# Performance work log

Hardware: AMD Instinct MI355X
Metric: run time of the kernel (lower is better)

Reference implementation:

```python
import jax, jax.numpy as jnp
import numpy as np
import math

MID = 48       # mid_channels
HEADS = 4      # num_heads
POS = 16       # mid_channels // 3 (row/col positional channels)


def _unfold(x, p):
    """nn.Unfold with kernel p, padding p//2: (..., H, W) -> (..., p, p, H, W)."""
    H, W = x.shape[-2], x.shape[-1]
    pad = p // 2
    xp = jnp.pad(x, [(0, 0)] * (x.ndim - 2) + [(pad, pad), (pad, pad)])
    return jnp.stack(
        [jnp.stack([xp[..., k:k + H, l:l + W] for l in range(p)], axis=-3)
         for k in range(p)], axis=-4)


def _pe_mlp(idx, w1, b1, g, b, w2, b2):
    """Conv2d(1->16,1x1) -> LayerNorm(16) -> Swish -> Conv2d(16->POS,1x1) on scalar coords."""
    t = idx.reshape(-1, 1)                         # (N,1)
    h = t @ w1.T + b1                              # (N,16)
    mu = jnp.mean(h, -1, keepdims=True)
    var = jnp.var(h, -1, keepdims=True)
    h = (h - mu) * jax.lax.rsqrt(var + 1e-5) * g + b
    h = h * jax.nn.sigmoid(h)                      # Swish
    e = h @ w2.T + b2                              # (N,POS)
    return e.reshape(idx.shape + (e.shape[-1],))   # (V,P,P,POS)


def setup_inputs() -> dict:
    key = jax.random.key(0)
    ks = jax.random.split(key, 32)
    B, Cin, G, H, W, P, Cout = 2, 32, 4, 28, 28, 7, 64

    def n(k, shp, s=0.05):
        return jax.random.normal(k, shp, dtype=jnp.float32) * s

    inp = {"x": jax.random.normal(ks[0], (B, Cin, G, H, W), dtype=jnp.float32)}
    inp["Wq"] = n(ks[1], (MID * HEADS, Cin)); inp["bq"] = n(ks[2], (MID * HEADS,))
    inp["Wk"] = n(ks[3], (MID * HEADS, Cin)); inp["bk"] = n(ks[4], (MID * HEADS,))
    inp["Wv"] = n(ks[5], (MID * HEADS, Cin)); inp["bv"] = n(ks[6], (MID * HEADS,))
    inp["Wout"] = n(ks[7], (Cout, MID * HEADS)); inp["bout"] = n(ks[8], (Cout,))
    inp["row_w1"] = n(ks[9], (16, 1)); inp["row_b1"] = n(ks[10], (16,))
    inp["row_ln_g"] = jnp.ones((16,), jnp.float32); inp["row_ln_b"] = jnp.zeros((16,), jnp.float32)
    inp["row_w2"] = n(ks[11], (POS, 16)); inp["row_b2"] = n(ks[12], (POS,))
    inp["col_w1"] = n(ks[13], (16, 1)); inp["col_b1"] = n(ks[14], (16,))
    inp["col_ln_g"] = jnp.ones((16,), jnp.float32); inp["col_ln_b"] = jnp.zeros((16,), jnp.float32)
    inp["col_w2"] = n(ks[15], (POS, 16)); inp["col_b2"] = n(ks[16], (POS,))
    inp["group_emb"] = n(ks[17], (G, MID - 2 * POS))
    # rotated relative spatial positions, normalized to [-1, 1]
    lin = np.linspace(-1.0, 1.0, P).astype(np.float32)
    r = np.repeat(lin[:, None], P, 1)
    c = np.repeat(lin[None, :], P, 0)
    rows, cols = [], []
    for v in range(G):
        th = v * math.pi / 2.0
        rows.append(math.cos(th) * r - math.sin(th) * c)
        cols.append(math.sin(th) * r + math.cos(th) * c)
    inp["row_indices"] = jnp.asarray(np.stack(rows, 0))
    inp["col_indices"] = jnp.asarray(np.stack(cols, 0))
    # acted relative group positions for cyclic group C4
    ar = np.arange(G)
    gi = (ar[:, None, None] + ar[None, None, :] - ar[None, :, None]) % G
    inp["g_indices"] = jnp.asarray(gi, dtype=jnp.int32)
    return inp


def _forward(x, Wq, bq, Wk, bk, Wv, bv, Wout, bout,
             row_w1, row_b1, row_ln_g, row_ln_b, row_w2, row_b2,
             col_w1, col_b1, col_ln_g, col_ln_b, col_w2, col_b2,
             group_emb, row_indices, col_indices, g_indices):
    B, Cin, G, H, W = x.shape
    P = row_indices.shape[-1]
    sqn = jnp.sqrt(jnp.float32(Cin))

    def proj(Wm, bm):  # 1x1 Conv3d -> (B, MID, HEADS, G, H, W)
        y = jnp.einsum('oi,bigyx->bogyx', Wm, x) + bm[None, :, None, None, None]
        return y.reshape(B, MID, HEADS, G, H, W)

    q = proj(Wq, bq)
    k = proj(Wk, bk)
    v = proj(Wv, bv)
    k_loc = _unfold(k, P)   # (B, MID, HEADS, G, P, P, H, W)
    v_loc = _unfold(v, P)

    content = jnp.einsum('bchgij,bchmklij->bhgijmkl', q, k_loc)
    row_e = _pe_mlp(row_indices, row_w1, row_b1, row_ln_g, row_ln_b, row_w2, row_b2)
    col_e = _pe_mlp(col_indices, col_w1, col_b1, col_ln_g, col_ln_b, col_w2, col_b2)
    row_s = jnp.einsum('bchgij,vklc->bhvgijkl', q[:, :POS], row_e)
    col_s = jnp.einsum('bchgij,vklc->bhvgijkl', q[:, POS:2 * POS], col_e)
    g_e = group_emb[g_indices]                              # (V, G, M, gdim)
    g_s = jnp.einsum('bchgij,vgmc->bhvgijm', q[:, 2 * POS:], g_e)

    # scores: (b, h, v, g, i, j, m, k, l)
    scores = (row_s[:, :, :, :, :, :, None] + col_s[:, :, :, :, :, :, None]
              + g_s[..., None, None] + content[:, :, None]) / sqn

    # mask patch positions that fall outside the image (-inf -> prob 0)
    valid = _unfold(jnp.ones((H, W), jnp.float32), P)       # (P, P, H, W)
    valid = jnp.transpose(valid, (2, 3, 0, 1))[None, None, None, None, :, :, None, :, :]
    scores = jnp.where(valid > 0.5, scores, -jnp.inf)

    shp = scores.shape
    probs = jax.nn.softmax(scores.reshape(shp[:-3] + (-1,)), axis=-1).reshape(shp)

    o = jnp.einsum('bhvgijmkl,bchmklij->bchvij', probs, v_loc)  # (B, MID, HEADS, V, H, W)
    o = o.reshape(B, MID * HEADS, G, H, W)
    return jnp.einsum('oi,bivyx->bovyx', Wout, o) + bout[None, :, None, None, None]


def reference(x, Wq, bq, Wk, bk, Wv, bv, Wout, bout,
              row_w1, row_b1, row_ln_g, row_ln_b, row_w2, row_b2,
              col_w1, col_b1, col_ln_g, col_ln_b, col_w2, col_b2,
              group_emb, row_indices, col_indices, g_indices):
    return _forward(x, Wq, bq, Wk, bk, Wv, bv, Wout, bout,
                    row_w1, row_b1, row_ln_g, row_ln_b, row_w2, row_b2,
                    col_w1, col_b1, col_ln_g, col_ln_b, col_w2, col_b2,
                    group_emb, row_indices, col_indices, g_indices)
```

## Files before the change

### kernel.cpp

```cpp
#include <hip/hip_runtime.h>
#include <math.h>

#define Bb   2
#define CIN  32
#define Gg   4
#define NH   4
#define Hh   28
#define Ww   28
#define HW   784
#define Pp   7
#define PP   49
#define MID  48
#define COUT 64
#define OC   192

#define QOFF  0
#define KOFF  1204224
#define VOFF  2408448
#define OOFF  3612672

#define KSCALE 0.2550611135387359f

#define VP1F 3360

__device__ unsigned g_peT2[Gg * PP * 16];
__device__ unsigned g_geT2[8 * 64];
__device__ float    g_WT2[OC * COUT];

typedef _Float16 h2f __attribute__((ext_vector_type(2)));

__device__ __forceinline__ unsigned packh2(float a, float b) {
    auto r = __builtin_amdgcn_cvt_pkrtz(a, b);
    return __builtin_bit_cast(unsigned, r);
}

__device__ __forceinline__ float fdot2(unsigned a, unsigned b, float c) {
    return __builtin_amdgcn_fdot2(__builtin_bit_cast(h2f, a),
                                  __builtin_bit_cast(h2f, b), c, false);
}

__device__ __forceinline__ float exp2_fast(float x) {
    float r;
    asm("v_exp_f32 %0, %1" : "=v"(r) : "v"(x));
    return r;
}

__global__ __launch_bounds__(192) void qkvpe_kernel(const float* __restrict__ x,
    const float* __restrict__ Wq, const float* __restrict__ bq,
    const float* __restrict__ Wk, const float* __restrict__ bk,
    const float* __restrict__ Wv, const float* __restrict__ bv,
    const float* row_w1, const float* row_b1,
    const float* row_g,  const float* row_bb,
    const float* row_w2, const float* row_b2,
    const float* col_w1, const float* col_b1,
    const float* col_g,  const float* col_bb,
    const float* col_w2, const float* col_b2,
    const float* row_idx, const float* col_idx,
    const float* group_emb, const int* g_indices,
    const float* Wout,
    float* __restrict__ ws)
{
    __shared__ float xs[CIN * 16];
    __shared__ float wtmp[16 * 193];
    int tid = threadIdx.x;
    if (blockIdx.x == Bb * Gg * Hh * 2) {
        for (int t = tid; t < 2 * Gg * PP; t += 192) {
            int half = t / (Gg * PP);
            int n    = t - half * (Gg * PP);
            int v = n / PP, kl = n % PP;
            const float* w1 = half ? col_w1 : row_w1;
            const float* b1 = half ? col_b1 : row_b1;
            const float* lg = half ? col_g  : row_g;
            const float* lb = half ? col_bb : row_bb;
            const float* w2 = half ? col_w2 : row_w2;
            const float* b2 = half ? col_b2 : row_b2;
            float tv = half ? col_idx[n] : row_idx[n];

            float hb[16];
            float mean = 0.f;
            for (int k = 0; k < 16; k++) { hb[k] = tv * w1[k] + b1[k]; mean += hb[k]; }
            mean *= (1.f / 16.f);
            float var = 0.f;
            for (int k = 0; k < 16; k++) { float d = hb[k] - mean; var += d * d; }
            var *= (1.f / 16.f);
            float inv = 1.f / sqrtf(var + 1e-5f);
            for (int k = 0; k < 16; k++) {
                float hn = (hb[k] - mean) * inv * lg[k] + lb[k];
                hb[k] = hn / (1.f + expf(-hn));
            }
            float accv[16];
            for (int p = 0; p < 16; p++) {
                float acc = b2[p];
                for (int k = 0; k < 16; k++) acc += hb[k] * w2[p * 16 + k];
                accv[p] = acc * KSCALE;
            }
            for (int i2 = 0; i2 < 8; i2++)
                g_peT2[(v * PP + kl) * 16 + half * 8 + i2] =
                    packh2(accv[2 * i2], accv[2 * i2 + 1]);
        }
        for (int t = tid; t < 64; t += 192) {
            int gi = g_indices[t];
            for (int i2 = 0; i2 < 8; i2++)
                g_geT2[i2 * 64 + t] = packh2(group_emb[gi * 16 + 2 * i2] * KSCALE,
                                             group_emb[gi * 16 + 2 * i2 + 1] * KSCALE);
        }
        for (int chunk = 0; chunk < 4; chunk++) {
            int obase = chunk * 16;
            __syncthreads();
            for (int idx = tid; idx < 16 * OC; idx += 192) {
                int ol = idx / OC, t = idx % OC;
                wtmp[ol * 193 + t] = Wout[(obase + ol) * OC + t];
            }
            __syncthreads();
            for (int idx = tid; idx < 16 * OC; idx += 192) {
                int tp = idx / 16, ol = idx % 16;
                int h = tp / MID, c = tp % MID;
                g_WT2[tp * 64 + obase + ol] = wtmp[ol * 193 + c * NH + h];
            }
        }
        return;
    }

    int r = blockIdx.x;
    int jh = r & 1; r >>= 1;
    int i = r % Hh; r /= Hh;
    int g = r & 3;  int b = r >> 2;
    int j0 = jh * 14;

    for (int idx = tid; idx < CIN * 14; idx += 192) {
        int ci = idx / 14, jj = idx % 14;
        xs[ci * 16 + jj] = x[((b * CIN + ci) * Gg + g) * HW + i * Ww + j0 + jj];
    }
    __syncthreads();

    int h = tid / MID, c = tid % MID;
    int oo = c * NH + h;
    int wbase = (((b * NH + h) * Gg + g) * HW + i * Ww + j0) * MID + c;

    const float* Wm[3]  = {Wq, Wk, Wv};
    const float* bm[3]  = {bq, bk, bv};
    const int    off[3] = {QOFF, KOFF, VOFF};
    const float  scl[3] = {1.0f, KSCALE, 1.0f};
    for (int p = 0; p < 3; p++) {
        const float4* Wr4 = (const float4*)(Wm[p] + oo * CIN);
        float bias = bm[p][oo];
        float a[14];
        #pragma unroll
        for (int j = 0; j < 14; j++) a[j] = bias;

        #pragma unroll 2
        for (int ci8 = 0; ci8 < 8; ci8++) {
            float4 wv4 = Wr4[ci8];
            int cb = ci8 * 4;
#define CHAN(WV, CI)                                                          \
            {                                                                 \
                float wv = WV;                                                \
                float4 xA = *(const float4*)&xs[(CI) * 16 + 0];               \
                float4 xB = *(const float4*)&xs[(CI) * 16 + 4];               \
                float4 xC = *(const float4*)&xs[(CI) * 16 + 8];               \
                float2 xD = *(const float2*)&xs[(CI) * 16 + 12];              \
                a[0] += wv * xA.x;  a[1] += wv * xA.y;                        \
                a[2] += wv * xA.z;  a[3] += wv * xA.w;                        \
                a[4] += wv * xB.x;  a[5] += wv * xB.y;                        \
                a[6] += wv * xB.z;  a[7] += wv * xB.w;                        \
                a[8] += wv * xC.x;  a[9] += wv * xC.y;                        \
                a[10] += wv * xC.z; a[11] += wv * xC.w;                       \
                a[12] += wv * xD.x; a[13] += wv * xD.y;                       \
            }
            CHAN(wv4.x, cb + 0)
            CHAN(wv4.y, cb + 1)
            CHAN(wv4.z, cb + 2)
            CHAN(wv4.w, cb + 3)
#undef CHAN
        }
        float s = scl[p];
        #pragma unroll
        for (int j = 0; j < 14; j++) ws[off[p] + wbase + j * MID] = a[j] * s;
    }
}

__global__ __launch_bounds__(256, 4) void attn_kernel(float* __restrict__ ws)
{
    __shared__ __align__(16) unsigned kvb[7560];
    __shared__ __align__(16) unsigned pp2[4][PP][8];
    __shared__ __align__(16) unsigned qp[4][4][32];
    __shared__ __align__(16) float gsm[4][64];

    const int tid  = threadIdx.x;
    const int wave = tid >> 6;
    const int lane = tid & 63;

    int blk = blockIdx.x;
    int j0 = (blk % 7) * 4;
    int i  = (blk / 7) % Hh;
    int bh = blk / (7 * Hh);
    int b = bh >> 2, h = bh & 3;
    int j  = j0 + wave;
    int ij = i * Ww + j;

    const float* Qt  = ws + QOFF;
    const float* Kbh = ws + KOFF + (size_t)bh * Gg * HW * MID;
    const float* Vbh = ws + VOFF + (size_t)bh * Gg * HW * MID;
    float* Ot = ws + OOFF;

    if (lane < 48) {
        int g = lane / 12, c4 = lane % 12;
        float4 qv = *(const float4*)&Qt[((size_t)(bh * Gg + g) * HW + ij) * MID + c4 * 4];
        qp[wave][g][c4 * 2]     = packh2(qv.x, qv.y);
        qp[wave][g][c4 * 2 + 1] = packh2(qv.z, qv.w);
    }

    #pragma unroll
    for (int s = 0; s < 4; s++) {
        int t = tid + s * 256;
        if (t < 840) {
            int c4 = t % 12, cl = t / 12;
            int gy = i - 3 + cl / 10, gx = j0 - 3 + cl % 10;
            bool ok = ((unsigned)gy < Hh) && ((unsigned)gx < Ww);
            const float* kp = &Kbh[(size_t)(gy * Ww + gx) * MID + c4 * 4];
            #pragma unroll
            for (int m = 0; m < 4; m++) {
                float4 val = {0.f, 0.f, 0.f, 0.f};
                if (ok) val = *(const float4*)(kp + (size_t)m * HW * MID);
                *(uint2*)&kvb[(m * 70 + cl) * 27 + c4 * 2] =
                    make_uint2(packh2(val.x, val.y), packh2(val.z, val.w));
            }
        }
    }

    int kk = lane / Pp, ll = lane % Pp;
    int cell = (lane < PP) ? kk * 10 + ll + wave : 0;
    bool vmask = (lane < PP) && ((unsigned)(i + kk - 3) < Hh) && ((unsigned)(j + ll - 3) < Ww);
    int lclamp = lane < PP ? lane : 0;

    float per[4][4] = {};
    #pragma unroll
    for (int u4 = 0; u4 < 4; u4++) {
        uint4 qA = *(const uint4*)&qp[wave][0][u4 * 4];
        uint4 qB = *(const uint4*)&qp[wave][1][u4 * 4];
        uint4 qC = *(const uint4*)&qp[wave][2][u4 * 4];
        uint4 qD = *(const uint4*)&qp[wave][3][u4 * 4];
        #pragma unroll
        for (int v = 0; v < 4; v++) {
            uint4 pk = *(const uint4*)&g_peT2[(v * PP + lclamp) * 16 + u4 * 4];
            per[v][0] = fdot2(pk.w, qA.w, fdot2(pk.z, qA.z, fdot2(pk.y, qA.y, fdot2(pk.x, qA.x, per[v][0]))));
            per[v][1] = fdot2(pk.w, qB.w, fdot2(pk.z, qB.z, fdot2(pk.y, qB.y, fdot2(pk.x, qB.x, per[v][1]))));
            per[v][2] = fdot2(pk.w, qC.w, fdot2(pk.z, qC.z, fdot2(pk.y, qC.y, fdot2(pk.x, qC.x, per[v][2]))));
            per[v][3] = fdot2(pk.w, qD.w, fdot2(pk.z, qD.z, fdot2(pk.y, qD.y, fdot2(pk.x, qD.x, per[v][3]))));
        }
    }
    if (!vmask) {
        #pragma unroll
        for (int v = 0; v < 4; v++)
            #pragma unroll
            for (int g = 0; g < 4; g++) per[v][g] = -INFINITY;
    }

    {
        int g = (lane >> 2) & 3;
        float ga = 0.f;
        #pragma unroll
        for (int u = 0; u < 8; u++)
            ga = fdot2(g_geT2[u * 64 + lane], qp[wave][g][16 + u], ga);
        gsm[wave][lane] = ga;
    }
    __syncthreads();

    float acc[4][4] = {};
    #pragma unroll 2
    for (int u4 = 0; u4 < 6; u4++) {
        uint4 qA = *(const uint4*)&qp[wave][0][u4 * 4];
        uint4 qB = *(const uint4*)&qp[wave][1][u4 * 4];
        uint4 qC = *(const uint4*)&qp[wave][2][u4 * 4];
        uint4 qD = *(const uint4*)&qp[wave][3][u4 * 4];
        #pragma unroll
        for (int m = 0; m < 4; m++) {
            int base = (m * 70 + cell) * 27 + u4 * 4;
            uint2 k01 = *(const uint2*)&kvb[base];
            uint2 k23 = *(const uint2*)&kvb[base + 2];
            acc[m][0] = fdot2(k23.y, qA.w, fdot2(k23.x, qA.z, fdot2(k01.y, qA.y, fdot2(k01.x, qA.x, acc[m][0]))));
            acc[m][1] = fdot2(k23.y, qB.w, fdot2(k23.x, qB.z, fdot2(k01.y, qB.y, fdot2(k01.x, qB.x, acc[m][1]))));
            acc[m][2] = fdot2(k23.y, qC.w, fdot2(k23.x, qC.z, fdot2(k01.y, qC.y, fdot2(k01.x, qC.x, acc[m][2]))));
            acc[m][3] = fdot2(k23.y, qD.w, fdot2(k23.x, qD.z, fdot2(k01.y, qD.y, fdot2(k01.x, qD.x, acc[m][3]))));
        }
    }

    float ppr[4][4] = {};
    #pragma unroll
    for (int v = 0; v < 4; v++) {
        #pragma unroll
        for (int g = 0; g < 4; g++) {
            int vg = v * 4 + g;
            float4 gs = *(const float4*)&gsm[wave][vg * 4];
            float ex[4];
            ex[0] = exp2_fast(acc[0][g] + per[v][g] + gs.x);
            ex[1] = exp2_fast(acc[1][g] + per[v][g] + gs.y);
            ex[2] = exp2_fast(acc[2][g] + per[v][g] + gs.z);
            ex[3] = exp2_fast(acc[3][g] + per[v][g] + gs.w);
            float ls = ex[0] + ex[1] + ex[2] + ex[3];
            #pragma unroll
            for (int d = 32; d > 0; d >>= 1) ls += __shfl_xor(ls, d, 64);
            float rinv = 1.0f / ls;
            #pragma unroll
            for (int m = 0; m < 4; m++) ppr[v][m] += ex[m] * rinv;
        }
    }
    if (lane < PP) {
        uint4 w0, w1;
        w0.x = packh2(ppr[0][0], ppr[0][1]); w0.y = packh2(ppr[0][2], ppr[0][3]);
        w0.z = packh2(ppr[1][0], ppr[1][1]); w0.w = packh2(ppr[1][2], ppr[1][3]);
        w1.x = packh2(ppr[2][0], ppr[2][1]); w1.y = packh2(ppr[2][2], ppr[2][3]);
        w1.z = packh2(ppr[3][0], ppr[3][1]); w1.w = packh2(ppr[3][2], ppr[3][3]);
        *(uint4*)&pp2[wave][lane][0] = w0;
        *(uint4*)&pp2[wave][lane][4] = w1;
    }
    __syncthreads();

    for (int t = tid; t < 840; t += 256) {
        int c4 = t % 12; int cl = t / 12;
        int gy = i - 3 + cl / 10, gx = j0 - 3 + cl % 10;
        float4 v0 = {0.f,0.f,0.f,0.f}, v1 = v0, v2 = v0, v3 = v0;
        if ((unsigned)gy < Hh && (unsigned)gx < Ww) {
            const float* vp = &Vbh[((size_t)(gy * Ww + gx)) * MID + c4 * 4];
            v0 = *(const float4*)vp;
            v1 = *(const float4*)(vp + (size_t)HW * MID);
            v2 = *(const float4*)(vp + (size_t)2 * HW * MID);
            v3 = *(const float4*)(vp + (size_t)3 * HW * MID);
        }
        uint4 wA, wB;
        wA.x = packh2(v0.x, v1.x); wA.y = packh2(v0.y, v1.y);
        wA.z = packh2(v0.z, v1.z); wA.w = packh2(v0.w, v1.w);
        wB.x = packh2(v2.x, v3.x); wB.y = packh2(v2.y, v3.y);
        wB.z = packh2(v2.z, v3.z); wB.w = packh2(v2.w, v3.w);
        *(uint4*)&kvb[cl * 48 + c4 * 4] = wA;
        *(uint4*)&kvb[VP1F + cl * 48 + c4 * 4] = wB;
    }
    __syncthreads();

    if (lane < MID) {
        float o0 = 0.f, o1 = 0.f, o2 = 0.f, o3 = 0.f;
        const uint4* ppw = (const uint4*)&pp2[wave][0][0];
        const unsigned* v0b = &kvb[wave * 48 + lane];
        const unsigned* v1b = v0b + VP1F;
        #pragma unroll
        for (int kl2 = 0; kl2 < PP; kl2++) {
            int cellc = (kl2 / Pp) * 10 + (kl2 % Pp);
            unsigned vv0 = v0b[cellc * 48];
            unsigned vv1 = v1b[cellc * 48];
            uint4 A = ppw[kl2 * 2];
            uint4 B = ppw[kl2 * 2 + 1];
            o0 = fdot2(vv1, A.y, fdot2(vv0, A.x, o0));
            o1 = fdot2(vv1, A.w, fdot2(vv0, A.z, o1));
            o2 = fdot2(vv1, B.y, fdot2(vv0, B.x, o2));
            o3 = fdot2(vv1, B.w, fdot2(vv0, B.z, o3));
        }
        Ot[((size_t)(b * Gg + 0) * HW + ij) * OC + h * MID + lane] = o0;
        Ot[((size_t)(b * Gg + 1) * HW + ij) * OC + h * MID + lane] = o1;
        Ot[((size_t)(b * Gg + 2) * HW + ij) * OC + h * MID + lane] = o2;
        Ot[((size_t)(b * Gg + 3) * HW + ij) * OC + h * MID + lane] = o3;
    }
}

__global__ __launch_bounds__(256) void outproj_kernel(const float* __restrict__ bout,
                                                      const float* __restrict__ ws,
                                                      float* __restrict__ out)
{
    __shared__ float ov[16 * 193];
    __shared__ float res[64 * 17];
    int tid = threadIdx.x;
    int p0 = blockIdx.x * 16;
    const float* Ot = ws + OOFF;

    for (int idx = tid; idx < 16 * OC; idx += 256) {
        int pl = idx / OC, t = idx % OC;
        ov[pl * 193 + t] = Ot[(size_t)(p0 + pl) * OC + t];
    }
    __syncthreads();

    int o = tid & 63, pg = tid >> 6;
    float a0 = bout[o], a1 = a0, a2 = a0, a3 = a0;
    for (int t = 0; t < OC; t++) {
        float w = g_WT2[t * 64 + o];
        a0 += w * ov[(pg     ) * 193 + t];
        a1 += w * ov[(pg +  4) * 193 + t];
        a2 += w * ov[(pg +  8) * 193 + t];
        a3 += w * ov[(pg + 12) * 193 + t];
    }
    res[o * 17 + pg     ] = a0;
    res[o * 17 + pg +  4] = a1;
    res[o * 17 + pg +  8] = a2;
    res[o * 17 + pg + 12] = a3;
    __syncthreads();

    for (int idx = tid; idx < 1024; idx += 256) {
        int o2 = idx >> 4, pl = idx & 15;
        int p = p0 + pl;
        int ij2 = p % HW; int bv = p / HW; int v = bv & 3; int bb = bv >> 2;
        out[((bb * COUT + o2) * Gg + v) * HW + ij2] = res[o2 * 17 + pl];
    }
}

extern "C" void kernel_launch(void* const* d_in, const int* in_sizes, int n_in,
                              void* d_out, int out_size, void* d_ws, size_t ws_size,
                              hipStream_t stream)
{
    const float* x      = (const float*)d_in[0];
    const float* Wq     = (const float*)d_in[1];
    const float* bq     = (const float*)d_in[2];
    const float* Wk     = (const float*)d_in[3];
    const float* bk     = (const float*)d_in[4];
    const float* Wv     = (const float*)d_in[5];
    const float* bv     = (const float*)d_in[6];
    const float* Wout   = (const float*)d_in[7];
    const float* bout   = (const float*)d_in[8];
    const float* row_w1 = (const float*)d_in[9];
    const float* row_b1 = (const float*)d_in[10];
    const float* row_g  = (const float*)d_in[11];
    const float* row_bb = (const float*)d_in[12];
    const float* row_w2 = (const float*)d_in[13];
    const float* row_b2 = (const float*)d_in[14];
    const float* col_w1 = (const float*)d_in[15];
    const float* col_b1 = (const float*)d_in[16];
    const float* col_g  = (const float*)d_in[17];
    const float* col_bb = (const float*)d_in[18];
    const float* col_w2 = (const float*)d_in[19];
    const float* col_b2 = (const float*)d_in[20];
    const float* gemb   = (const float*)d_in[21];
    const float* ridx   = (const float*)d_in[22];
    const float* cidx   = (const float*)d_in[23];
    const int*   gidx   = (const int*)d_in[24];

    float* ws  = (float*)d_ws;
    float* out = (float*)d_out;

    qkvpe_kernel<<<Bb * Gg * Hh * 2 + 1, 192, 0, stream>>>(
        x, Wq, bq, Wk, bk, Wv, bv,
        row_w1, row_b1, row_g, row_bb, row_w2, row_b2,
        col_w1, col_b1, col_g, col_bb, col_w2, col_b2,
        ridx, cidx, gemb, gidx, Wout, ws);
    attn_kernel<<<Bb * NH * Hh * (Ww / 4), 256, 0, stream>>>(ws);
    outproj_kernel<<<Bb * Gg * HW / 16, 256, 0, stream>>>(bout, ws, out);
}
```

Before: 175.6 us.

## Store Q/K/V workspace as packed fp16 and prefetch V tiles before softmax

```diff
diff --git a/kernel.cpp b/kernel.cpp
--- a/kernel.cpp
+++ b/kernel.cpp
@@ -14,14 +14,16 @@
 #define COUT 64
 #define OC   192
 
-#define QOFF  0
-#define KOFF  1204224
-#define VOFF  2408448
-#define OOFF  3612672
+#define QF    0
+#define KF    602112
+#define VF    1204224
+#define OOFF  1806336
+#define KBH   75264
+#define KM    18816
+#define VBH   75264
+#define VPL   37632
 
 #define KSCALE 0.2550611135387359f
-
-#define VP1F 3360
 
 __device__ unsigned g_peT2[Gg * PP * 16];
 __device__ unsigned g_geT2[8 * 64];
@@ -43,6 +45,37 @@
     float r;
     asm("v_exp_f32 %0, %1" : "=v"(r) : "v"(x));
     return r;
+}
+
+__device__ __forceinline__ void conv14(const float4* __restrict__ Wr4, float bias,
+                                       const float* __restrict__ xr, float* a) {
+    #pragma unroll
+    for (int j = 0; j < 14; j++) a[j] = bias;
+    #pragma unroll 2
+    for (int ci8 = 0; ci8 < 8; ci8++) {
+        float4 wv4 = Wr4[ci8];
+        int cb = ci8 * 4;
+#define CHAN(WV, CI)                                                          \
+        {                                                                     \
+            float wv = WV;                                                    \
+            float4 xA = *(const float4*)&xr[(CI) * 16 + 0];                   \
+            float4 xB = *(const float4*)&xr[(CI) * 16 + 4];                   \
+            float4 xC = *(const float4*)&xr[(CI) * 16 + 8];                   \
+            float2 xD = *(const float2*)&xr[(CI) * 16 + 12];                  \
+            a[0] += wv * xA.x;  a[1] += wv * xA.y;                            \
+            a[2] += wv * xA.z;  a[3] += wv * xA.w;                            \
+            a[4] += wv * xB.x;  a[5] += wv * xB.y;                            \
+            a[6] += wv * xB.z;  a[7] += wv * xB.w;                            \
+            a[8] += wv * xC.x;  a[9] += wv * xC.y;                            \
+            a[10] += wv * xC.z; a[11] += wv * xC.w;                           \
+            a[12] += wv * xD.x; a[13] += wv * xD.y;                           \
+        }
+        CHAN(wv4.x, cb + 0)
+        CHAN(wv4.y, cb + 1)
+        CHAN(wv4.z, cb + 2)
+        CHAN(wv4.w, cb + 3)
+#undef CHAN
+    }
 }
 
 __global__ __launch_bounds__(192) void qkvpe_kernel(const float* __restrict__ x,
@@ -60,10 +93,11 @@
     const float* Wout,
     float* __restrict__ ws)
 {
-    __shared__ float xs[CIN * 16];
+    __shared__ float xs[2 * CIN * 16];
     __shared__ float wtmp[16 * 193];
     int tid = threadIdx.x;
-    if (blockIdx.x == Bb * Gg * Hh * 2) {
+    unsigned* uw = (unsigned*)ws;
+    if (blockIdx.x == Bb * 2 * Hh * 2) {
         for (int t = tid; t < 2 * Gg * PP; t += 192) {
             int half = t / (Gg * PP);
             int n    = t - half * (Gg * PP);
@@ -124,64 +158,59 @@
     int r = blockIdx.x;
     int jh = r & 1; r >>= 1;
     int i = r % Hh; r /= Hh;
-    int g = r & 3;  int b = r >> 2;
+    int gp = r & 1; int b = r >> 1;
     int j0 = jh * 14;
 
-    for (int idx = tid; idx < CIN * 14; idx += 192) {
-        int ci = idx / 14, jj = idx % 14;
-        xs[ci * 16 + jj] = x[((b * CIN + ci) * Gg + g) * HW + i * Ww + j0 + jj];
+    for (int idx = tid; idx < 2 * CIN * 14; idx += 192) {
+        int gs = idx / (CIN * 14), rem = idx % (CIN * 14);
+        int ci = rem / 14, jj = rem % 14;
+        xs[gs * CIN * 16 + ci * 16 + jj] =
+            x[((b * CIN + ci) * Gg + 2 * gp + gs) * HW + i * Ww + j0 + jj];
     }
     __syncthreads();
 
     int h = tid / MID, c = tid % MID;
     int oo = c * NH + h;
-    int wbase = (((b * NH + h) * Gg + g) * HW + i * Ww + j0) * MID + c;
-
-    const float* Wm[3]  = {Wq, Wk, Wv};
-    const float* bm[3]  = {bq, bk, bv};
-    const int    off[3] = {QOFF, KOFF, VOFF};
-    const float  scl[3] = {1.0f, KSCALE, 1.0f};
-    for (int p = 0; p < 3; p++) {
-        const float4* Wr4 = (const float4*)(Wm[p] + oo * CIN);
-        float bias = bm[p][oo];
-        float a[14];
-        #pragma unroll
-        for (int j = 0; j < 14; j++) a[j] = bias;
-
-        #pragma unroll 2
-        for (int ci8 = 0; ci8 < 8; ci8++) {
-            float4 wv4 = Wr4[ci8];
-            int cb = ci8 * 4;
-#define CHAN(WV, CI)                                                          \
-            {                                                                 \
-                float wv = WV;                                                \
-                float4 xA = *(const float4*)&xs[(CI) * 16 + 0];               \
-                float4 xB = *(const float4*)&xs[(CI) * 16 + 4];               \
-                float4 xC = *(const float4*)&xs[(CI) * 16 + 8];               \
-                float2 xD = *(const float2*)&xs[(CI) * 16 + 12];              \
-                a[0] += wv * xA.x;  a[1] += wv * xA.y;                        \
-                a[2] += wv * xA.z;  a[3] += wv * xA.w;                        \
-                a[4] += wv * xB.x;  a[5] += wv * xB.y;                        \
-                a[6] += wv * xB.z;  a[7] += wv * xB.w;                        \
-                a[8] += wv * xC.x;  a[9] += wv * xC.y;                        \
-                a[10] += wv * xC.z; a[11] += wv * xC.w;                       \
-                a[12] += wv * xD.x; a[13] += wv * xD.y;                       \
-            }
-            CHAN(wv4.x, cb + 0)
-            CHAN(wv4.y, cb + 1)
-            CHAN(wv4.z, cb + 2)
-            CHAN(wv4.w, cb + 3)
-#undef CHAN
-        }
-        float s = scl[p];
-        #pragma unroll
-        for (int j = 0; j < 14; j++) ws[off[p] + wbase + j * MID] = a[j] * s;
+    int bh = b * NH + h;
+    int ij0 = i * Ww + j0;
+
+    #pragma unroll 1
+    for (int p = 0; p < 2; p++) {
+        const float* Wm = p ? Wk : Wq;
+        const float* bm = p ? bk : bq;
+        float scl = p ? KSCALE : 1.0f;
+        int base0 = p ? KF : QF;
+        const float4* Wr4 = (const float4*)(Wm + oo * CIN);
+        float bias = bm[oo];
+        #pragma unroll 1
+        for (int gs = 0; gs < 2; gs++) {
+            float a[14];
+            conv14(Wr4, bias, &xs[gs * CIN * 16], a);
+            int obase = base0 + ((bh * Gg + 2 * gp + gs) * HW + ij0) * 24 + (c >> 1);
+            #pragma unroll
+            for (int jj = 0; jj < 14; jj++) {
+                float av = a[jj] * scl;
+                float pr = __shfl_xor(av, 1, 64);
+                if (!(tid & 1)) uw[obase + jj * 24] = packh2(av, pr);
+            }
+        }
+    }
+    {
+        const float4* Wr4 = (const float4*)(Wv + oo * CIN);
+        float bias = bv[oo];
+        float a0[14], a1[14];
+        conv14(Wr4, bias, &xs[0], a0);
+        conv14(Wr4, bias, &xs[CIN * 16], a1);
+        int obase = VF + ((bh * 2 + gp) * HW + ij0) * 48 + c;
+        #pragma unroll
+        for (int jj = 0; jj < 14; jj++)
+            uw[obase + jj * 48] = packh2(a0[jj], a1[jj]);
     }
 }
 
 __global__ __launch_bounds__(256, 4) void attn_kernel(float* __restrict__ ws)
 {
-    __shared__ __align__(16) unsigned kvb[7560];
+    __shared__ __align__(16) unsigned kvb[7000];
     __shared__ __align__(16) unsigned pp2[4][PP][8];
     __shared__ __align__(16) unsigned qp[4][4][32];
     __shared__ __align__(16) float gsm[4][64];
@@ -198,32 +227,32 @@
     int j  = j0 + wave;
     int ij = i * Ww + j;
 
-    const float* Qt  = ws + QOFF;
-    const float* Kbh = ws + KOFF + (size_t)bh * Gg * HW * MID;
-    const float* Vbh = ws + VOFF + (size_t)bh * Gg * HW * MID;
+    const unsigned* uw = (const unsigned*)ws;
+    const unsigned* Kf = uw + KF + bh * KBH;
+    const unsigned* Vf = uw + VF + bh * VBH;
     float* Ot = ws + OOFF;
 
     if (lane < 48) {
         int g = lane / 12, c4 = lane % 12;
-        float4 qv = *(const float4*)&Qt[((size_t)(bh * Gg + g) * HW + ij) * MID + c4 * 4];
-        qp[wave][g][c4 * 2]     = packh2(qv.x, qv.y);
-        qp[wave][g][c4 * 2 + 1] = packh2(qv.z, qv.w);
+        uint2 qv = *(const uint2*)&uw[QF + ((bh * Gg + g) * HW + ij) * 24 + c4 * 2];
+        qp[wave][g][c4 * 2]     = qv.x;
+        qp[wave][g][c4 * 2 + 1] = qv.y;
     }
 
     #pragma unroll
-    for (int s = 0; s < 4; s++) {
+    for (int s = 0; s < 2; s++) {
         int t = tid + s * 256;
-        if (t < 840) {
-            int c4 = t % 12, cl = t / 12;
+        if (t < 420) {
+            int c8 = t % 6, cl = t / 6;
             int gy = i - 3 + cl / 10, gx = j0 - 3 + cl % 10;
-            bool ok = ((unsigned)gy < Hh) && ((unsigned)gx < Ww);
-            const float* kp = &Kbh[(size_t)(gy * Ww + gx) * MID + c4 * 4];
+            gy = min(max(gy, 0), Hh - 1); gx = min(max(gx, 0), Ww - 1);
+            const unsigned* kp = &Kf[(gy * Ww + gx) * 24 + c8 * 4];
             #pragma unroll
             for (int m = 0; m < 4; m++) {
-                float4 val = {0.f, 0.f, 0.f, 0.f};
-                if (ok) val = *(const float4*)(kp + (size_t)m * HW * MID);
-                *(uint2*)&kvb[(m * 70 + cl) * 27 + c4 * 2] =
-                    make_uint2(packh2(val.x, val.y), packh2(val.z, val.w));
+                uint4 kv = *(const uint4*)(kp + m * KM);
+                int o = (m * 70 + cl) * 25 + c8 * 4;
+                *(uint2*)&kvb[o]     = make_uint2(kv.x, kv.y);
+                *(uint2*)&kvb[o + 2] = make_uint2(kv.z, kv.w);
             }
         }
     }
@@ -275,7 +304,7 @@
         uint4 qD = *(const uint4*)&qp[wave][3][u4 * 4];
         #pragma unroll
         for (int m = 0; m < 4; m++) {
-            int base = (m * 70 + cell) * 27 + u4 * 4;
+            int base = (m * 70 + cell) * 25 + u4 * 4;
             uint2 k01 = *(const uint2*)&kvb[base];
             uint2 k23 = *(const uint2*)&kvb[base + 2];
             acc[m][0] = fdot2(k23.y, qA.w, fdot2(k23.x, qA.z, fdot2(k01.y, qA.y, fdot2(k01.x, qA.x, acc[m][0]))));
@@ -284,6 +313,23 @@
             acc[m][3] = fdot2(k23.y, qD.w, fdot2(k23.x, qD.z, fdot2(k01.y, qD.y, fdot2(k01.x, qD.x, acc[m][3]))));
         }
     }
+
+#define VLOAD(T, A, Bv)                                                       \
+    {   int c4_ = (T) % 12, cl_ = (T) / 12;                                   \
+        int gy_ = i - 3 + cl_ / 10, gx_ = j0 - 3 + cl_ % 10;                  \
+        gy_ = min(max(gy_, 0), Hh - 1); gx_ = min(max(gx_, 0), Ww - 1);       \
+        int off_ = (gy_ * Ww + gx_) * 48 + c4_ * 4;                           \
+        A  = *(const uint4*)&Vf[off_];                                        \
+        Bv = *(const uint4*)&Vf[VPL + off_]; }
+#define VSTORE(T, A, Bv)                                                      \
+    {   int c4_ = (T) % 12, cl_ = (T) / 12;                                   \
+        int o_ = cl_ * 48 + c4_ * 4;                                          \
+        *(uint4*)&kvb[o_]        = A;                                         \
+        *(uint4*)&kvb[3360 + o_] = Bv; }
+    uint4 pA0, pB0, pA1, pB1, pA2, pB2;
+    VLOAD(tid,       pA0, pB0)
+    VLOAD(tid + 256, pA1, pB1)
+    VLOAD(tid + 512, pA2, pB2)
 
     float ppr[4][4] = {};
     #pragma unroll
@@ -316,32 +362,21 @@
     }
     __syncthreads();
 
-    for (int t = tid; t < 840; t += 256) {
-        int c4 = t % 12; int cl = t / 12;
-        int gy = i - 3 + cl / 10, gx = j0 - 3 + cl % 10;
-        float4 v0 = {0.f,0.f,0.f,0.f}, v1 = v0, v2 = v0, v3 = v0;
-        if ((unsigned)gy < Hh && (unsigned)gx < Ww) {
-            const float* vp = &Vbh[((size_t)(gy * Ww + gx)) * MID + c4 * 4];
-            v0 = *(const float4*)vp;
-            v1 = *(const float4*)(vp + (size_t)HW * MID);
-            v2 = *(const float4*)(vp + (size_t)2 * HW * MID);
-            v3 = *(const float4*)(vp + (size_t)3 * HW * MID);
-        }
-        uint4 wA, wB;
-        wA.x = packh2(v0.x, v1.x); wA.y = packh2(v0.y, v1.y);
-        wA.z = packh2(v0.z, v1.z); wA.w = packh2(v0.w, v1.w);
-        wB.x = packh2(v2.x, v3.x); wB.y = packh2(v2.y, v3.y);
-        wB.z = packh2(v2.z, v3.z); wB.w = packh2(v2.w, v3.w);
-        *(uint4*)&kvb[cl * 48 + c4 * 4] = wA;
-        *(uint4*)&kvb[VP1F + cl * 48 + c4 * 4] = wB;
-    }
+    uint4 sA, sB;
+    if (tid < 72) { VLOAD(tid + 768, sA, sB) }
+    VSTORE(tid,       pA0, pB0)
+    VSTORE(tid + 256, pA1, pB1)
+    VSTORE(tid + 512, pA2, pB2)
+    if (tid < 72) { VSTORE(tid + 768, sA, sB) }
+#undef VLOAD
+#undef VSTORE
     __syncthreads();
 
     if (lane < MID) {
         float o0 = 0.f, o1 = 0.f, o2 = 0.f, o3 = 0.f;
         const uint4* ppw = (const uint4*)&pp2[wave][0][0];
         const unsigned* v0b = &kvb[wave * 48 + lane];
-        const unsigned* v1b = v0b + VP1F;
+        const unsigned* v1b = v0b + 3360;
         #pragma unroll
         for (int kl2 = 0; kl2 < PP; kl2++) {
             int cellc = (kl2 / Pp) * 10 + (kl2 % Pp);
@@ -433,7 +468,7 @@
     float* ws  = (float*)d_ws;
     float* out = (float*)d_out;
 
-    qkvpe_kernel<<<Bb * Gg * Hh * 2 + 1, 192, 0, stream>>>(
+    qkvpe_kernel<<<Bb * 2 * Hh * 2 + 1, 192, 0, stream>>>(
         x, Wq, bq, Wk, bk, Wv, bv,
         row_w1, row_b1, row_g, row_bb, row_w2, row_b2,
         col_w1, col_b1, col_g, col_bb, col_w2, col_b2,
```

Measured after the change: 169.0 us. -3.8%, faster.
